# Kernel tuning notes

Hardware: AMD Instinct MI355X
Metric: run time of the kernel (lower is better)

Reference implementation:

```python
import jax, jax.numpy as jnp
import numpy as np

B, T, IDIM = 16, 1024, 345
L, D, H, DK, FF = 4, 256, 4, 64, 1024
EPS = 1e-5


def layer_norm(x, s, b):
    m = jnp.mean(x, axis=-1, keepdims=True)
    v = jnp.mean(jnp.square(x - m), axis=-1, keepdims=True)
    return (x - m) * jax.lax.rsqrt(v + EPS) * s + b


def setup_inputs() -> dict:
    key = jax.random.key(0)
    ks = jax.random.split(key, 16)
    w = 0.02
    return {
        "x": jax.random.normal(ks[0], (B, T, IDIM), jnp.float32),
        "num_frames": int(T),
        "Win": w * jax.random.normal(ks[1], (IDIM, D), jnp.float32),
        "b_in": jnp.zeros((D,), jnp.float32),
        "ln1_s": jnp.ones((L, D), jnp.float32),
        "ln1_b": jnp.zeros((L, D), jnp.float32),
        "Wq": w * jax.random.normal(ks[2], (L, D, D), jnp.float32),
        "bq": jnp.zeros((L, D), jnp.float32),
        "Wk": w * jax.random.normal(ks[3], (L, D, D), jnp.float32),
        "bk": jnp.zeros((L, D), jnp.float32),
        "Wv": w * jax.random.normal(ks[4], (L, D, D), jnp.float32),
        "bv": jnp.zeros((L, D), jnp.float32),
        "Wo": w * jax.random.normal(ks[5], (L, D, D), jnp.float32),
        "bo": jnp.zeros((L, D), jnp.float32),
        "ln2_s": jnp.ones((L, D), jnp.float32),
        "ln2_b": jnp.zeros((L, D), jnp.float32),
        "W1": w * jax.random.normal(ks[6], (L, D, FF), jnp.float32),
        "b1": jnp.zeros((L, FF), jnp.float32),
        "W2": w * jax.random.normal(ks[7], (L, FF, D), jnp.float32),
        "b2": jnp.zeros((L, D), jnp.float32),
        "lno_s": jnp.ones((D,), jnp.float32),
        "lno_b": jnp.zeros((D,), jnp.float32),
    }


def reference(x, num_frames, Win, b_in, ln1_s, ln1_b, Wq, bq, Wk, bk, Wv, bv,
              Wo, bo, ln2_s, ln2_b, W1, b1, W2, b2, lno_s, lno_b):
    num = x.shape[0]
    scale = 1.0 / np.sqrt(DK)
    # [num*T, D]
    e = x.reshape(-1, x.shape[-1]) @ Win + b_in
    for i in range(L):
        e = layer_norm(e, ln1_s[i], ln1_b[i])
        # naive MHSA (residual taken from LN output, as in the source)
        q = (e @ Wq[i] + bq[i]).reshape(num, -1, H, DK)
        k = (e @ Wk[i] + bk[i]).reshape(num, -1, H, DK)
        v = (e @ Wv[i] + bv[i]).reshape(num, -1, H, DK)
        scores = jnp.einsum('bqhd,bkhd->bhqk', q, k) * scale
        attn = jax.nn.softmax(scores, axis=-1)
        o = jnp.einsum('bhqk,bkhd->bqhd', attn, v).reshape(-1, D)
        e = e + (o @ Wo[i] + bo[i])
        e = layer_norm(e, ln2_s[i], ln2_b[i])
        e = e + (jax.nn.relu(e @ W1[i] + b1[i]) @ W2[i] + b2[i])
    out = layer_norm(e, lno_s, lno_b)
    return out.reshape(num, num_frames, -1)
```

## Files before the change

### kernel.cpp

```cpp
#include <hip/hip_runtime.h>
#include <hip/hip_bf16.h>

#define BB    16
#define TT    1024
#define MTOK  (BB*TT)
#define IDIM_ 345
#define KPAD  384
#define LL    4
#define DD_   256
#define FF_   1024
#define EPS_  1e-5f
#define QSCL  0.18033688f

typedef __bf16 bf16;
typedef bf16 bf16x8 __attribute__((ext_vector_type(8)));
typedef float f32x4 __attribute__((ext_vector_type(4)));

static __device__ __forceinline__ f32x4 MFMA(bf16x8 a, bf16x8 b, f32x4 c) {
  return __builtin_amdgcn_mfma_f32_16x16x32_bf16(a, b, c, 0, 0, 0);
}
static __device__ __forceinline__ unsigned bfbits(float x) {
  return (unsigned)__builtin_bit_cast(unsigned short, (bf16)x);
}
static __device__ __forceinline__ bf16x8 ld_bf8(const void* p) {
  return *reinterpret_cast<const bf16x8*>(p);
}
static __device__ __forceinline__ void gload_lds16(const bf16* g, void* l) {
  __builtin_amdgcn_global_load_lds(
      (const __attribute__((address_space(1))) void*)g,
      (__attribute__((address_space(3))) void*)l, 16, 0, 0);
}

__global__ void k_convert_pad(const float* __restrict__ src, bf16* __restrict__ dst) {
  int idx = blockIdx.x * 256 + threadIdx.x;
  if (idx >= MTOK * (KPAD / 4)) return;
  int r = idx / (KPAD / 4), c0 = (idx % (KPAD / 4)) * 4;
  const float* s = src + (long)r * IDIM_ + c0;
  float v0 = (c0 + 0 < IDIM_) ? s[0] : 0.f;
  float v1 = (c0 + 1 < IDIM_) ? s[1] : 0.f;
  float v2 = (c0 + 2 < IDIM_) ? s[2] : 0.f;
  float v3 = (c0 + 3 < IDIM_) ? s[3] : 0.f;
  uint2 pk;
  pk.x = bfbits(v0) | (bfbits(v1) << 16);
  pk.y = bfbits(v2) | (bfbits(v3) << 16);
  *reinterpret_cast<uint2*>(dst + (long)r * KPAD + c0) = pk;
}

__global__ void k_wt_convert(const float* __restrict__ src, bf16* __restrict__ dst,
                             int K, int N, int Kp) {
  int idx = blockIdx.x * 256 + threadIdx.x;
  if (idx >= N * Kp) return;
  int n = idx / Kp, kk = idx % Kp;
  dst[idx] = (kk < K) ? (bf16)src[(long)kk * N + n] : (bf16)0.f;
}

__global__ __launch_bounds__(256)
void k_wt_all(const float* __restrict__ Wq, const float* __restrict__ Wk,
              const float* __restrict__ Wv, const float* __restrict__ Wo,
              const float* __restrict__ W1, const float* __restrict__ W2,
              bf16* __restrict__ Wqkvt, bf16* __restrict__ Wot,
              bf16* __restrict__ W1t, bf16* __restrict__ W2t) {
  __shared__ float tile[64][65];
  const int s = blockIdx.y, m = s >> 2, i = s & 3;
  const float* src; bf16* dst; int K, N;
  switch (m) {
    case 0: src = Wq + (long)i*65536;  dst = Wqkvt + (long)i*196608;          K=256;  N=256;  break;
    case 1: src = Wk + (long)i*65536;  dst = Wqkvt + (long)i*196608 + 65536;  K=256;  N=256;  break;
    case 2: src = Wv + (long)i*65536;  dst = Wqkvt + (long)i*196608 + 131072; K=256;  N=256;  break;
    case 3: src = Wo + (long)i*65536;  dst = Wot + (long)i*65536;             K=256;  N=256;  break;
    case 4: src = W1 + (long)i*262144; dst = W1t + (long)i*262144;            K=256;  N=1024; break;
    default:src = W2 + (long)i*262144; dst = W2t + (long)i*262144;            K=1024; N=256;  break;
  }
  const int tiles_n = N >> 6, ntiles = (K >> 6) * tiles_n;
  if (blockIdx.x >= ntiles) return;
  const int tk = blockIdx.x / tiles_n, tn = blockIdx.x % tiles_n;
  const int t = threadIdx.x, rq = t >> 6, cl = t & 63;
  #pragma unroll
  for (int i2 = 0; i2 < 16; i2++)
    tile[rq * 16 + i2][cl] = src[(long)(tk * 64 + rq * 16 + i2) * N + tn * 64 + cl];
  __syncthreads();
  #pragma unroll
  for (int i2 = 0; i2 < 16; i2++)
    dst[(long)(tn * 64 + rq * 16 + i2) * K + tk * 64 + cl] = (bf16)tile[cl][rq * 16 + i2];
}

__global__ void k_bias_concat(const float* __restrict__ bq, const float* __restrict__ bk,
                              const float* __restrict__ bv, float* __restrict__ bqkv) {
  int idx = blockIdx.x * 256 + threadIdx.x;
  if (idx >= LL * 768) return;
  int i = idx / 768, j = idx % 768;
  float v = (j < 256) ? bq[i*256 + j] : (j < 512 ? bk[i*256 + j - 256] : bv[i*256 + j - 512]);
  bqkv[idx] = v;
}

__global__ __launch_bounds__(256)
void k_ln(const float* __restrict__ in, float* __restrict__ outf,
          bf16* __restrict__ outb, const float* __restrict__ s,
          const float* __restrict__ b) {
  const int wave = threadIdx.x >> 6, lane = threadIdx.x & 63;
  const int row = blockIdx.x * 4 + wave;
  const float4 xv = *reinterpret_cast<const float4*>(in + (long)row * DD_ + lane * 4);
  float sum = xv.x + xv.y + xv.z + xv.w;
  #pragma unroll
  for (int off = 1; off < 64; off <<= 1) sum += __shfl_xor(sum, off);
  const float m = sum * (1.f / DD_);
  const float dx = xv.x - m, dy = xv.y - m, dz = xv.z - m, dw = xv.w - m;
  float ss = dx*dx + dy*dy + dz*dz + dw*dw;
  #pragma unroll
  for (int off = 1; off < 64; off <<= 1) ss += __shfl_xor(ss, off);
  const float inv = rsqrtf(ss * (1.f / DD_) + EPS_);
  const float4 sv = *reinterpret_cast<const float4*>(s + lane * 4);
  const float4 bv = *reinterpret_cast<const float4*>(b + lane * 4);
  float4 y;
  y.x = dx * inv * sv.x + bv.x;
  y.y = dy * inv * sv.y + bv.y;
  y.z = dz * inv * sv.z + bv.z;
  y.w = dw * inv * sv.w + bv.w;
  if (outf) *reinterpret_cast<float4*>(outf + (long)row * DD_ + lane * 4) = y;
  if (outb) {
    uint2 pk;
    pk.x = bfbits(y.x) | (bfbits(y.y) << 16);
    pk.y = bfbits(y.z) | (bfbits(y.w) << 16);
    *reinterpret_cast<uint2*>(outb + (long)row * DD_ + lane * 4) = pk;
  }
}

__global__ __launch_bounds__(256)
void k_gemm(const bf16* __restrict__ A, const bf16* __restrict__ Wt,
            const float* __restrict__ bias, const bf16* __restrict__ resid,
            float* __restrict__ out, int M, int N, int K) {
  __shared__ alignas(16) char As[2][8192];
  __shared__ alignas(16) char Bs[2][8192];
  const int t = threadIdx.x, lane = t & 63, wid = t >> 6;
  const int wr = wid >> 1, wc = wid & 1;
  const int g = lane >> 4, c = lane & 15;
  int flat = blockIdx.y * gridDim.x + blockIdx.x;
  const int cpx = (gridDim.x * gridDim.y) >> 3;
  flat = (flat & 7) * cpx + (flat >> 3);
  const int mbase = (flat / gridDim.x) * 64, nbase = (flat % gridDim.x) * 64;

  const int srow = t >> 3;
  const int skc = (((t & 7) ^ (srow & 7)) * 8);
  const bf16* ag = A  + (long)(mbase + srow) * K + skc;
  const bf16* bg = Wt + (long)(nbase + srow) * K + skc;
  const int swz = (c & 7) << 4;

  f32x4 acc[2][2] = {};

#define GSTAGE(bi, k0) do { \
    gload_lds16(ag + (k0),                  As[bi] + wid * 1024); \
    gload_lds16(ag + (k0) + 32 * (long)K,   As[bi] + 4096 + wid * 1024); \
    gload_lds16(bg + (k0),                  Bs[bi] + wid * 1024); \
    gload_lds16(bg + (k0) + 32 * (long)K,   Bs[bi] + 4096 + wid * 1024); \
  } while (0)

  const int nk = K >> 6;
  GSTAGE(0, 0);
  int cur = 0;
  for (int kt = 0; kt < nk; ++kt) {
    if (kt + 1 < nk) {
      GSTAGE(cur ^ 1, (kt + 1) * 64);
      asm volatile("s_waitcnt vmcnt(4)" ::: "memory");
    } else {
      asm volatile("s_waitcnt vmcnt(0)" ::: "memory");
    }
    __builtin_amdgcn_s_barrier();

    bf16x8 af[2][2], bfr[2][2];
    #pragma unroll
    for (int mi = 0; mi < 2; mi++)
      #pragma unroll
      for (int ks = 0; ks < 2; ks++)
        af[mi][ks] = ld_bf8(As[cur] + (wr * 32 + mi * 16 + c) * 128 + ((ks * 64 + g * 16) ^ swz));
    #pragma unroll
    for (int ni = 0; ni < 2; ni++)
      #pragma unroll
      for (int ks = 0; ks < 2; ks++)
        bfr[ni][ks] = ld_bf8(Bs[cur] + (wc * 32 + ni * 16 + c) * 128 + ((ks * 64 + g * 16) ^ swz));
    __builtin_amdgcn_s_setprio(1);
    #pragma unroll
    for (int mi = 0; mi < 2; mi++)
      #pragma unroll
      for (int ni = 0; ni < 2; ni++)
        #pragma unroll
        for (int ks = 0; ks < 2; ks++)
          acc[mi][ni] = MFMA(af[mi][ks], bfr[ni][ks], acc[mi][ni]);
    __builtin_amdgcn_s_setprio(0);
    __builtin_amdgcn_s_barrier();
    cur ^= 1;
  }
#undef GSTAGE

  #pragma unroll
  for (int mi = 0; mi < 2; mi++) {
    #pragma unroll
    for (int ni = 0; ni < 2; ni++) {
      const int colg = nbase + wc * 32 + ni * 16 + c;
      const float bv = bias ? bias[colg] : 0.f;
      #pragma unroll
      for (int j = 0; j < 4; j++) {
        const int rowg = mbase + wr * 32 + mi * 16 + g * 4 + j;
        float r = resid ? (float)resid[(long)rowg * N + colg] : 0.f;
        out[(long)rowg * N + colg] = r + acc[mi][ni][j] + bv;
      }
    }
  }
}

template<int EPI>
__global__ __launch_bounds__(256)
void k_gemm_big(const bf16* __restrict__ A, const bf16* __restrict__ Wt,
                const float* __restrict__ bias, void* __restrict__ out,
                bf16* __restrict__ vt, int N, int K) {
  __shared__ alignas(16) char As[16384];
  __shared__ alignas(16) char Bs[16384];
  const int t = threadIdx.x, lane = t & 63, wid = t >> 6;
  const int wr = wid >> 1, wc = wid & 1;
  const int g = lane >> 4, c = lane & 15;
  int flat = blockIdx.y * gridDim.x + blockIdx.x;
  const int cpx = (gridDim.x * gridDim.y) >> 3;
  flat = (flat & 7) * cpx + (flat >> 3);
  const int mbase = (flat / gridDim.x) * 128, nbase = (flat % gridDim.x) * 128;

  const int srow = t >> 3;
  const int skc = ((t & 7) ^ (srow & 7)) * 8;
  const bf16* ag = A  + (long)(mbase + srow) * K + skc;
  const bf16* bg = Wt + (long)(nbase + srow) * K + skc;
  const int swz = (c & 7) << 4;

  f32x4 acc[4][4] = {};

  const int nk = K >> 6;
  for (int kt = 0; kt < nk; ++kt) {
    const int k0 = kt * 64;
    __syncthreads();
    #pragma unroll
    for (int p = 0; p < 4; p++) {
      gload_lds16(ag + (long)p * 32 * K + k0, As + p * 4096 + wid * 1024);
      gload_lds16(bg + (long)p * 32 * K + k0, Bs + p * 4096 + wid * 1024);
    }
    __syncthreads();

    bf16x8 af[4][2], bfr[4][2];
    #pragma unroll
    for (int mi = 0; mi < 4; mi++)
      #pragma unroll
      for (int ks = 0; ks < 2; ks++)
        af[mi][ks] = ld_bf8(As + (wr * 64 + mi * 16 + c) * 128 + ((ks * 64 + g * 16) ^ swz));
    #pragma unroll
    for (int ni = 0; ni < 4; ni++)
      #pragma unroll
      for (int ks = 0; ks < 2; ks++)
        bfr[ni][ks] = ld_bf8(Bs + (wc * 64 + ni * 16 + c) * 128 + ((ks * 64 + g * 16) ^ swz));
    __builtin_amdgcn_s_setprio(1);
    #pragma unroll
    for (int mi = 0; mi < 4; mi++)
      #pragma unroll
      for (int ni = 0; ni < 4; ni++)
        #pragma unroll
        for (int ks = 0; ks < 2; ks++)
          acc[mi][ni] = MFMA(af[mi][ks], bfr[ni][ks], acc[mi][ni]);
    __builtin_amdgcn_s_setprio(0);
  }

  #pragma unroll
  for (int mi = 0; mi < 4; mi++) {
    #pragma unroll
    for (int ni = 0; ni < 4; ni++) {
      const int colg = nbase + wc * 64 + ni * 16 + c;
      const float bv = bias ? bias[colg] : 0.f;
      if constexpr (EPI == 3) {
        if (nbase < 512) {
          const float qs = (nbase < 256) ? QSCL : 1.0f;
          #pragma unroll
          for (int j = 0; j < 4; j++) {
            const int rowg = mbase + wr * 64 + mi * 16 + g * 4 + j;
            ((bf16*)out)[(long)rowg * N + colg] = (bf16)((acc[mi][ni][j] + bv) * qs);
          }
        } else {
          const int dfull = colg - 512, hh = dfull >> 6, d = dfull & 63;
          const int rowg0 = mbase + wr * 64 + mi * 16 + g * 4;
          uint2 st;
          st.x = bfbits(acc[mi][ni][0] + bv) | (bfbits(acc[mi][ni][1] + bv) << 16);
          st.y = bfbits(acc[mi][ni][2] + bv) | (bfbits(acc[mi][ni][3] + bv) << 16);
          *reinterpret_cast<uint2*>(vt + (long)(((rowg0 >> 10) << 2) + hh) * 65536
                                       + d * 1024 + (rowg0 & 1023)) = st;
        }
      } else {
        #pragma unroll
        for (int j = 0; j < 4; j++) {
          const int rowg = mbase + wr * 64 + mi * 16 + g * 4 + j;
          ((bf16*)out)[(long)rowg * N + colg] = (bf16)fmaxf(acc[mi][ni][j] + bv, 0.f);
        }
      }
    }
  }
}

__global__ __launch_bounds__(256)
void k_attn(const bf16* __restrict__ qkv, const bf16* __restrict__ vtg,
            bf16* __restrict__ o) {
  __shared__ alignas(16) char Ks[2][8192];
  __shared__ alignas(16) char Vs[2][8192];
  __shared__ alignas(16) char Ps[16384];
  const int t = threadIdx.x, lane = t & 63, w = t >> 6;
  const int g = lane >> 4, c = lane & 15;
  int flat = blockIdx.y * 8 + blockIdx.x;
  flat = (flat & 7) * 64 + (flat >> 3);
  const int bh = flat >> 3, qt = flat & 7;
  const int b = bh >> 2, h = bh & 3;
  const long tokbase = (long)b * TT;
  const int qA = qt * 128 + w * 16 + c;
  const int qB = qA + 64;

  bf16x8 qf0A = ld_bf8(qkv + (tokbase + qA) * 768 + h * 64 + g * 8);
  bf16x8 qf1A = ld_bf8(qkv + (tokbase + qA) * 768 + h * 64 + 32 + g * 8);
  bf16x8 qf0B = ld_bf8(qkv + (tokbase + qB) * 768 + h * 64 + g * 8);
  bf16x8 qf1B = ld_bf8(qkv + (tokbase + qB) * 768 + h * 64 + 32 + g * 8);

  const int sr = t >> 3;
  const int slot = (t & 7) ^ (sr & 7);
  const int swz_c = (c & 7) << 4;
  const bf16* kbase = qkv + 256 + h * 64 + slot * 8;
  const bf16* vbase = vtg + (long)bh * 65536 + slot * 8;
  char* pwA = Ps + w * 4096 + c * 128;
  char* pwB = pwA + 2048;

#define KSTAGE(bi, jt) do { \
    gload_lds16(kbase + (tokbase + (jt) * 64 + sr) * 768,      Ks[bi] + w * 1024); \
    gload_lds16(kbase + (tokbase + (jt) * 64 + sr + 32) * 768, Ks[bi] + 4096 + w * 1024); \
    gload_lds16(vbase + (long)sr * 1024 + (jt) * 64,           Vs[bi] + w * 1024); \
    gload_lds16(vbase + (long)(sr + 32) * 1024 + (jt) * 64,    Vs[bi] + 4096 + w * 1024); \
  } while (0)

  f32x4 oaccA[4] = {}, oaccB[4] = {};
  float mrunA = -1e30f, lrunA = 0.f, mrunB = -1e30f, lrunB = 0.f;

  KSTAGE(0, 0);
  int cur = 0;
  for (int jt = 0; jt < 16; ++jt) {
    if (jt + 1 < 16) {
      KSTAGE(cur ^ 1, jt + 1);
      asm volatile("s_waitcnt vmcnt(4)" ::: "memory");
    } else {
      asm volatile("s_waitcnt vmcnt(0)" ::: "memory");
    }
    __builtin_amdgcn_s_barrier();

    f32x4 saccA[4] = {}, saccB[4] = {};
    __builtin_amdgcn_s_setprio(1);
    #pragma unroll
    for (int ni = 0; ni < 4; ni++) {
      const char* krow = Ks[cur] + (ni * 16 + c) * 128;
      bf16x8 kf0 = ld_bf8(krow + ((g * 16) ^ swz_c));
      bf16x8 kf1 = ld_bf8(krow + ((64 + g * 16) ^ swz_c));
      saccA[ni] = MFMA(kf0, qf0A, saccA[ni]);
      saccB[ni] = MFMA(kf0, qf0B, saccB[ni]);
      saccA[ni] = MFMA(kf1, qf1A, saccA[ni]);
      saccB[ni] = MFMA(kf1, qf1B, saccB[ni]);
    }
    __builtin_amdgcn_s_setprio(0);

    float mA = -1e30f, mB = -1e30f;
    #pragma unroll
    for (int ni = 0; ni < 4; ni++)
      #pragma unroll
      for (int j = 0; j < 4; j++) {
        mA = fmaxf(mA, saccA[ni][j]);
        mB = fmaxf(mB, saccB[ni][j]);
      }
    mA = fmaxf(mA, __shfl_xor(mA, 16));
    mB = fmaxf(mB, __shfl_xor(mB, 16));
    mA = fmaxf(mA, __shfl_xor(mA, 32));
    mB = fmaxf(mB, __shfl_xor(mB, 32));

    if (!__all(mA <= mrunA + 11.5f)) {
      const float mn = fmaxf(mrunA, mA);
      const float al = __builtin_amdgcn_exp2f(mrunA - mn);
      mrunA = mn; lrunA *= al;
      #pragma unroll
      for (int nd = 0; nd < 4; nd++)
        #pragma unroll
        for (int j = 0; j < 4; j++) oaccA[nd][j] *= al;
    }
    if (!__all(mB <= mrunB + 11.5f)) {
      const float mn = fmaxf(mrunB, mB);
      const float al = __builtin_amdgcn_exp2f(mrunB - mn);
      mrunB = mn; lrunB *= al;
      #pragma unroll
      for (int nd = 0; nd < 4; nd++)
        #pragma unroll
        for (int j = 0; j < 4; j++) oaccB[nd][j] *= al;
    }

    float rsA = 0.f, rsB = 0.f;
    #pragma unroll
    for (int ni = 0; ni < 4; ni++) {
      float a0 = __builtin_amdgcn_exp2f(saccA[ni][0] - mrunA);
      float b0 = __builtin_amdgcn_exp2f(saccB[ni][0] - mrunB);
      float a1 = __builtin_amdgcn_exp2f(saccA[ni][1] - mrunA);
      float b1 = __builtin_amdgcn_exp2f(saccB[ni][1] - mrunB);
      float a2 = __builtin_amdgcn_exp2f(saccA[ni][2] - mrunA);
      float b2 = __builtin_amdgcn_exp2f(saccB[ni][2] - mrunB);
      float a3 = __builtin_amdgcn_exp2f(saccA[ni][3] - mrunA);
      float b3 = __builtin_amdgcn_exp2f(saccB[ni][3] - mrunB);
      rsA += (a0 + a1) + (a2 + a3);
      rsB += (b0 + b1) + (b2 + b3);
      uint2 qa, qb;
      qa.x = bfbits(a0) | (bfbits(a1) << 16);
      qa.y = bfbits(a2) | (bfbits(a3) << 16);
      qb.x = bfbits(b0) | (bfbits(b1) << 16);
      qb.y = bfbits(b2) | (bfbits(b3) << 16);
      *reinterpret_cast<uint2*>(pwA + ((ni * 32 + g * 8) ^ swz_c)) = qa;
      *reinterpret_cast<uint2*>(pwB + ((ni * 32 + g * 8) ^ swz_c)) = qb;
    }
    rsA += __shfl_xor(rsA, 16);
    rsB += __shfl_xor(rsB, 16);
    rsA += __shfl_xor(rsA, 32);
    rsB += __shfl_xor(rsB, 32);
    lrunA += rsA;
    lrunB += rsB;

    __builtin_amdgcn_s_setprio(1);
    #pragma unroll
    for (int kk = 0; kk < 2; kk++) {
      bf16x8 pfA = ld_bf8(pwA + ((kk * 64 + g * 16) ^ swz_c));
      bf16x8 pfB = ld_bf8(pwB + ((kk * 64 + g * 16) ^ swz_c));
      #pragma unroll
      for (int nd = 0; nd < 4; nd++) {
        bf16x8 vf = ld_bf8(Vs[cur] + (nd * 16 + c) * 128 + ((kk * 64 + g * 16) ^ swz_c));
        oaccA[nd] = MFMA(vf, pfA, oaccA[nd]);
        oaccB[nd] = MFMA(vf, pfB, oaccB[nd]);
      }
    }
    __builtin_amdgcn_s_setprio(0);
    __builtin_amdgcn_s_barrier();
    cur ^= 1;
  }
#undef KSTAGE

  const float invA = 1.f / lrunA, invB = 1.f / lrunB;
  bf16* orowA = o + (tokbase + qA) * 256 + h * 64 + g * 4;
  bf16* orowB = o + (tokbase + qB) * 256 + h * 64 + g * 4;
  #pragma unroll
  for (int nd = 0; nd < 4; nd++) {
    uint2 sa, sb;
    sa.x = bfbits(oaccA[nd][0] * invA) | (bfbits(oaccA[nd][1] * invA) << 16);
    sa.y = bfbits(oaccA[nd][2] * invA) | (bfbits(oaccA[nd][3] * invA) << 16);
    sb.x = bfbits(oaccB[nd][0] * invB) | (bfbits(oaccB[nd][1] * invB) << 16);
    sb.y = bfbits(oaccB[nd][2] * invB) | (bfbits(oaccB[nd][3] * invB) << 16);
    *reinterpret_cast<uint2*>(orowA + nd * 16) = sa;
    *reinterpret_cast<uint2*>(orowB + nd * 16) = sb;
  }
}

extern "C" void kernel_launch(void* const* d_in, const int* in_sizes, int n_in,
                              void* d_out, int out_size, void* d_ws, size_t ws_size,
                              hipStream_t stream) {
  const float* x     = (const float*)d_in[0];
  const float* Win   = (const float*)d_in[2];
  const float* b_in  = (const float*)d_in[3];
  const float* ln1_s = (const float*)d_in[4];
  const float* ln1_b = (const float*)d_in[5];
  const float* Wq    = (const float*)d_in[6];
  const float* bq    = (const float*)d_in[7];
  const float* Wk    = (const float*)d_in[8];
  const float* bk    = (const float*)d_in[9];
  const float* Wv    = (const float*)d_in[10];
  const float* bv    = (const float*)d_in[11];
  const float* Wo    = (const float*)d_in[12];
  const float* bo    = (const float*)d_in[13];
  const float* ln2_s = (const float*)d_in[14];
  const float* ln2_b = (const float*)d_in[15];
  const float* W1    = (const float*)d_in[16];
  const float* b1    = (const float*)d_in[17];
  const float* W2    = (const float*)d_in[18];
  const float* b2    = (const float*)d_in[19];
  const float* lno_s = (const float*)d_in[20];
  const float* lno_b = (const float*)d_in[21];
  float* out = (float*)d_out;

  char* ws = (char*)d_ws;
  size_t off = 0;
  auto alloc = [&](size_t bytes) -> void* {
    void* p = ws + off; off += (bytes + 255) & ~(size_t)255; return p;
  };
  float* e    = (float*)alloc((size_t)MTOK * DD_ * 4);
  bf16* e_bf  = (bf16*)alloc((size_t)MTOK * DD_ * 2);
  bf16* qkvb  = (bf16*)alloc((size_t)MTOK * 768 * 2);
  bf16* vtb   = (bf16*)alloc((size_t)MTOK * DD_ * 2);
  bf16* ob    = (bf16*)alloc((size_t)MTOK * DD_ * 2);
  bf16* hb    = (bf16*)alloc((size_t)MTOK * FF_ * 2);
  bf16* x_bf  = (bf16*)hb;
  bf16* Wint  = (bf16*)alloc((size_t)DD_ * KPAD * 2);
  bf16* Wqkvt = (bf16*)alloc((size_t)LL * 768 * DD_ * 2);
  bf16* Wot   = (bf16*)alloc((size_t)LL * DD_ * DD_ * 2);
  bf16* W1t   = (bf16*)alloc((size_t)LL * DD_ * FF_ * 2);
  bf16* W2t   = (bf16*)alloc((size_t)LL * FF_ * DD_ * 2);
  float* bqkv = (float*)alloc((size_t)LL * 768 * 4);

  dim3 blk(256);

  k_convert_pad<<<(MTOK * (KPAD / 4) + 255) / 256, 256, 0, stream>>>(x, x_bf);
  k_wt_convert<<<(DD_ * KPAD + 255) / 256, 256, 0, stream>>>(Win, Wint, IDIM_, DD_, KPAD);
  k_wt_all<<<dim3(64, 24), blk, 0, stream>>>(Wq, Wk, Wv, Wo, W1, W2, Wqkvt, Wot, W1t, W2t);
  k_bias_concat<<<(LL * 768 + 255) / 256, 256, 0, stream>>>(bq, bk, bv, bqkv);

  k_gemm<<<dim3(4, 256), blk, 0, stream>>>(x_bf, Wint, b_in, nullptr, e, MTOK, DD_, KPAD);

  const long DDW = (long)DD_ * DD_;
  const long DFF = (long)DD_ * FF_;
  for (int i = 0; i < LL; i++) {
    k_ln<<<MTOK / 4, 256, 0, stream>>>(e, nullptr, e_bf, ln1_s + i * DD_, ln1_b + i * DD_);
    k_gemm_big<3><<<dim3(6, 128), blk, 0, stream>>>(e_bf, Wqkvt + (long)i * 768 * DD_,
                                                    bqkv + i * 768, qkvb, vtb, 768, DD_);
    k_attn<<<dim3(8, 64), blk, 0, stream>>>(qkvb, vtb, ob);
    k_gemm<<<dim3(4, 256), blk, 0, stream>>>(ob, Wot + i * DDW, bo + i * DD_, e_bf, e, MTOK, DD_, DD_);
    k_ln<<<MTOK / 4, 256, 0, stream>>>(e, nullptr, e_bf, ln2_s + i * DD_, ln2_b + i * DD_);
    k_gemm_big<1><<<dim3(8, 128), blk, 0, stream>>>(e_bf, W1t + i * DFF, b1 + i * FF_,
                                                    hb, nullptr, FF_, DD_);
    k_gemm<<<dim3(4, 256), blk, 0, stream>>>(hb, W2t + i * DFF, b2 + i * DD_, e_bf, e, MTOK, DD_, FF_);
  }
  k_ln<<<MTOK / 4, 256, 0, stream>>>(e, out, nullptr, lno_s, lno_b);
}
```

Measured before the change: 510.1 us.

## Fuse LayerNorm into full-row N=256 GEMM epilogues and drop fp32 residual buffer

Replaces the 64x64-tiled GEMM plus separate LayerNorm kernels with a GEMM whose blocks each own 32 full rows of 256 columns. Per-row mean and variance are reduced across waves through shared memory in the epilogue, and the normalized bf16 result is written directly. This removes nine standalone LN launches and the fp32 activation round-trip through memory. In exchange, the K loop loses its double-buffered prefetch and syncs twice per step, the grid is only 512 large blocks, and variance is now computed as E[x^2]-mean^2.

```diff
diff --git a/kernel.cpp b/kernel.cpp
--- a/kernel.cpp
+++ b/kernel.cpp
@@ -93,115 +93,110 @@
   bqkv[idx] = v;
 }
 
-__global__ __launch_bounds__(256)
-void k_ln(const float* __restrict__ in, float* __restrict__ outf,
-          bf16* __restrict__ outb, const float* __restrict__ s,
-          const float* __restrict__ b) {
-  const int wave = threadIdx.x >> 6, lane = threadIdx.x & 63;
-  const int row = blockIdx.x * 4 + wave;
-  const float4 xv = *reinterpret_cast<const float4*>(in + (long)row * DD_ + lane * 4);
-  float sum = xv.x + xv.y + xv.z + xv.w;
-  #pragma unroll
-  for (int off = 1; off < 64; off <<= 1) sum += __shfl_xor(sum, off);
-  const float m = sum * (1.f / DD_);
-  const float dx = xv.x - m, dy = xv.y - m, dz = xv.z - m, dw = xv.w - m;
-  float ss = dx*dx + dy*dy + dz*dz + dw*dw;
-  #pragma unroll
-  for (int off = 1; off < 64; off <<= 1) ss += __shfl_xor(ss, off);
-  const float inv = rsqrtf(ss * (1.f / DD_) + EPS_);
-  const float4 sv = *reinterpret_cast<const float4*>(s + lane * 4);
-  const float4 bv = *reinterpret_cast<const float4*>(b + lane * 4);
-  float4 y;
-  y.x = dx * inv * sv.x + bv.x;
-  y.y = dy * inv * sv.y + bv.y;
-  y.z = dz * inv * sv.z + bv.z;
-  y.w = dw * inv * sv.w + bv.w;
-  if (outf) *reinterpret_cast<float4*>(outf + (long)row * DD_ + lane * 4) = y;
-  if (outb) {
-    uint2 pk;
-    pk.x = bfbits(y.x) | (bfbits(y.y) << 16);
-    pk.y = bfbits(y.z) | (bfbits(y.w) << 16);
-    *reinterpret_cast<uint2*>(outb + (long)row * DD_ + lane * 4) = pk;
-  }
-}
-
-__global__ __launch_bounds__(256)
-void k_gemm(const bf16* __restrict__ A, const bf16* __restrict__ Wt,
-            const float* __restrict__ bias, const bf16* __restrict__ resid,
-            float* __restrict__ out, int M, int N, int K) {
-  __shared__ alignas(16) char As[2][8192];
-  __shared__ alignas(16) char Bs[2][8192];
+template<int EPI>
+__global__ __launch_bounds__(512, 4)
+void k_gemm_row(const bf16* __restrict__ A, const bf16* __restrict__ Wt,
+                const float* __restrict__ bias, const bf16* __restrict__ resid,
+                const float* __restrict__ lns, const float* __restrict__ lnb,
+                void* __restrict__ out, int K) {
+  __shared__ alignas(16) char As[4096];
+  __shared__ alignas(16) char Bs[32768];
+  __shared__ alignas(16) float redS[32][4];
+  __shared__ alignas(16) float redQ[32][4];
   const int t = threadIdx.x, lane = t & 63, wid = t >> 6;
-  const int wr = wid >> 1, wc = wid & 1;
+  const int wr = wid >> 2, wc = wid & 3;
   const int g = lane >> 4, c = lane & 15;
-  int flat = blockIdx.y * gridDim.x + blockIdx.x;
-  const int cpx = (gridDim.x * gridDim.y) >> 3;
-  flat = (flat & 7) * cpx + (flat >> 3);
-  const int mbase = (flat / gridDim.x) * 64, nbase = (flat % gridDim.x) * 64;
+  int flat = blockIdx.x;
+  flat = (flat & 7) * 64 + (flat >> 3);
+  const int mbase = flat * 32;
 
   const int srow = t >> 3;
-  const int skc = (((t & 7) ^ (srow & 7)) * 8);
-  const bf16* ag = A  + (long)(mbase + srow) * K + skc;
-  const bf16* bg = Wt + (long)(nbase + srow) * K + skc;
+  const int slot = ((t & 7) ^ (srow & 7)) * 8;
+  const bf16* ag = A  + (long)(mbase + srow) * K + slot;
+  const bf16* bg = Wt + (long)srow * K + slot;
   const int swz = (c & 7) << 4;
 
-  f32x4 acc[2][2] = {};
-
-#define GSTAGE(bi, k0) do { \
-    gload_lds16(ag + (k0),                  As[bi] + wid * 1024); \
-    gload_lds16(ag + (k0) + 32 * (long)K,   As[bi] + 4096 + wid * 1024); \
-    gload_lds16(bg + (k0),                  Bs[bi] + wid * 1024); \
-    gload_lds16(bg + (k0) + 32 * (long)K,   Bs[bi] + 4096 + wid * 1024); \
-  } while (0)
+  f32x4 acc[4] = {};
 
   const int nk = K >> 6;
-  GSTAGE(0, 0);
-  int cur = 0;
   for (int kt = 0; kt < nk; ++kt) {
-    if (kt + 1 < nk) {
-      GSTAGE(cur ^ 1, (kt + 1) * 64);
-      asm volatile("s_waitcnt vmcnt(4)" ::: "memory");
-    } else {
-      asm volatile("s_waitcnt vmcnt(0)" ::: "memory");
-    }
-    __builtin_amdgcn_s_barrier();
-
-    bf16x8 af[2][2], bfr[2][2];
-    #pragma unroll
-    for (int mi = 0; mi < 2; mi++)
+    const int k0 = kt * 64;
+    __syncthreads();
+    if (wid < 4) gload_lds16(ag + k0, As + wid * 1024);
+    #pragma unroll
+    for (int p = 0; p < 4; p++)
+      gload_lds16(bg + (long)(p * 64) * K + k0, Bs + p * 8192 + wid * 1024);
+    __syncthreads();
+
+    bf16x8 af[2], bfr[4][2];
+    #pragma unroll
+    for (int ks = 0; ks < 2; ks++)
+      af[ks] = ld_bf8(As + (wr * 16 + c) * 128 + ((ks * 64 + g * 16) ^ swz));
+    #pragma unroll
+    for (int ni = 0; ni < 4; ni++)
       #pragma unroll
       for (int ks = 0; ks < 2; ks++)
-        af[mi][ks] = ld_bf8(As[cur] + (wr * 32 + mi * 16 + c) * 128 + ((ks * 64 + g * 16) ^ swz));
-    #pragma unroll
-    for (int ni = 0; ni < 2; ni++)
+        bfr[ni][ks] = ld_bf8(Bs + (wc * 64 + ni * 16 + c) * 128 + ((ks * 64 + g * 16) ^ swz));
+    __builtin_amdgcn_s_setprio(1);
+    #pragma unroll
+    for (int ni = 0; ni < 4; ni++)
       #pragma unroll
       for (int ks = 0; ks < 2; ks++)
-        bfr[ni][ks] = ld_bf8(Bs[cur] + (wc * 32 + ni * 16 + c) * 128 + ((ks * 64 + g * 16) ^ swz));
-    __builtin_amdgcn_s_setprio(1);
-    #pragma unroll
-    for (int mi = 0; mi < 2; mi++)
-      #pragma unroll
-      for (int ni = 0; ni < 2; ni++)
-        #pragma unroll
-        for (int ks = 0; ks < 2; ks++)
-          acc[mi][ni] = MFMA(af[mi][ks], bfr[ni][ks], acc[mi][ni]);
+        acc[ni] = MFMA(af[ks], bfr[ni][ks], acc[ni]);
     __builtin_amdgcn_s_setprio(0);
-    __builtin_amdgcn_s_barrier();
-    cur ^= 1;
-  }
-#undef GSTAGE
-
-  #pragma unroll
-  for (int mi = 0; mi < 2; mi++) {
-    #pragma unroll
-    for (int ni = 0; ni < 2; ni++) {
-      const int colg = nbase + wc * 32 + ni * 16 + c;
-      const float bv = bias ? bias[colg] : 0.f;
-      #pragma unroll
-      for (int j = 0; j < 4; j++) {
-        const int rowg = mbase + wr * 32 + mi * 16 + g * 4 + j;
-        float r = resid ? (float)resid[(long)rowg * N + colg] : 0.f;
-        out[(long)rowg * N + colg] = r + acc[mi][ni][j] + bv;
+  }
+
+  float v[4][4];
+  float sP[4] = {0.f, 0.f, 0.f, 0.f}, qP[4] = {0.f, 0.f, 0.f, 0.f};
+  #pragma unroll
+  for (int ni = 0; ni < 4; ni++) {
+    const int col = wc * 64 + ni * 16 + c;
+    const float bb = bias[col];
+    #pragma unroll
+    for (int j = 0; j < 4; j++) {
+      const int row = mbase + wr * 16 + g * 4 + j;
+      float r = resid ? (float)resid[(long)row * 256 + col] : 0.f;
+      float x = acc[ni][j] + bb + r;
+      v[ni][j] = x;
+      sP[j] += x;
+      qP[j] += x * x;
+    }
+  }
+  #pragma unroll
+  for (int j = 0; j < 4; j++) {
+    #pragma unroll
+    for (int off = 1; off < 16; off <<= 1) {
+      sP[j] += __shfl_xor(sP[j], off);
+      qP[j] += __shfl_xor(qP[j], off);
+    }
+  }
+  if (c == 0) {
+    #pragma unroll
+    for (int j = 0; j < 4; j++) {
+      const int rb = wr * 16 + g * 4 + j;
+      redS[rb][wc] = sP[j];
+      redQ[rb][wc] = qP[j];
+    }
+  }
+  __syncthreads();
+
+  #pragma unroll
+  for (int j = 0; j < 4; j++) {
+    const int rb = wr * 16 + g * 4 + j;
+    const float4 s4 = *reinterpret_cast<const float4*>(redS[rb]);
+    const float4 q4 = *reinterpret_cast<const float4*>(redQ[rb]);
+    const float mean = (s4.x + s4.y + s4.z + s4.w) * (1.f / 256.f);
+    const float var = (q4.x + q4.y + q4.z + q4.w) * (1.f / 256.f) - mean * mean;
+    const float rstd = rsqrtf(var + EPS_);
+    const long row = mbase + wr * 16 + g * 4 + j;
+    #pragma unroll
+    for (int ni = 0; ni < 4; ni++) {
+      const int col = wc * 64 + ni * 16 + c;
+      const float y = (v[ni][j] - mean) * rstd * lns[col] + lnb[col];
+      if constexpr (EPI == 0) {
+        ((bf16*)out)[row * 256 + col] = (bf16)y;
+      } else {
+        ((float*)out)[row * 256 + col] = y;
       }
     }
   }
@@ -485,7 +480,6 @@
   auto alloc = [&](size_t bytes) -> void* {
     void* p = ws + off; off += (bytes + 255) & ~(size_t)255; return p;
   };
-  float* e    = (float*)alloc((size_t)MTOK * DD_ * 4);
   bf16* e_bf  = (bf16*)alloc((size_t)MTOK * DD_ * 2);
   bf16* qkvb  = (bf16*)alloc((size_t)MTOK * 768 * 2);
   bf16* vtb   = (bf16*)alloc((size_t)MTOK * DD_ * 2);
@@ -506,20 +500,26 @@
   k_wt_all<<<dim3(64, 24), blk, 0, stream>>>(Wq, Wk, Wv, Wo, W1, W2, Wqkvt, Wot, W1t, W2t);
   k_bias_concat<<<(LL * 768 + 255) / 256, 256, 0, stream>>>(bq, bk, bv, bqkv);
 
-  k_gemm<<<dim3(4, 256), blk, 0, stream>>>(x_bf, Wint, b_in, nullptr, e, MTOK, DD_, KPAD);
+  k_gemm_row<0><<<512, 512, 0, stream>>>(x_bf, Wint, b_in, nullptr,
+                                         ln1_s, ln1_b, e_bf, KPAD);
 
   const long DDW = (long)DD_ * DD_;
   const long DFF = (long)DD_ * FF_;
   for (int i = 0; i < LL; i++) {
-    k_ln<<<MTOK / 4, 256, 0, stream>>>(e, nullptr, e_bf, ln1_s + i * DD_, ln1_b + i * DD_);
     k_gemm_big<3><<<dim3(6, 128), blk, 0, stream>>>(e_bf, Wqkvt + (long)i * 768 * DD_,
                                                     bqkv + i * 768, qkvb, vtb, 768, DD_);
     k_attn<<<dim3(8, 64), blk, 0, stream>>>(qkvb, vtb, ob);
-    k_gemm<<<dim3(4, 256), blk, 0, stream>>>(ob, Wot + i * DDW, bo + i * DD_, e_bf, e, MTOK, DD_, DD_);
-    k_ln<<<MTOK / 4, 256, 0, stream>>>(e, nullptr, e_bf, ln2_s + i * DD_, ln2_b + i * DD_);
+    k_gemm_row<0><<<512, 512, 0, stream>>>(ob, Wot + i * DDW, bo + i * DD_, e_bf,
+                                           ln2_s + i * DD_, ln2_b + i * DD_, e_bf, DD_);
     k_gemm_big<1><<<dim3(8, 128), blk, 0, stream>>>(e_bf, W1t + i * DFF, b1 + i * FF_,
                                                     hb, nullptr, FF_, DD_);
-    k_gemm<<<dim3(4, 256), blk, 0, stream>>>(hb, W2t + i * DFF, b2 + i * DD_, e_bf, e, MTOK, DD_, FF_);
-  }
-  k_ln<<<MTOK / 4, 256, 0, stream>>>(e, out, nullptr, lno_s, lno_b);
-}
+    if (i < LL - 1) {
+      k_gemm_row<0><<<512, 512, 0, stream>>>(hb, W2t + i * DFF, b2 + i * DD_, e_bf,
+                                             ln1_s + (i + 1) * DD_, ln1_b + (i + 1) * DD_,
+                                             e_bf, FF_);
+    } else {
+      k_gemm_row<1><<<512, 512, 0, stream>>>(hb, W2t + i * DFF, b2 + i * DD_, e_bf,
+                                             lno_s, lno_b, out, FF_);
+    }
+  }
+}
```

New measurement: 445.6 us. -12.7%, faster.
